# Performance work log

Measured on AMD Instinct MI355X. Metric: run time of the kernel, lower is better.

The kernel has to match this reference:

```python
import math
import jax, jax.numpy as jnp
import numpy as np

D_MODEL = 1024
HEAD_DIM = 64  # D_MODEL // NUM_HEADS
B, T = 8, 2048


def setup_inputs() -> dict:
    key = jax.random.key(0)
    k1, k2, k3, k4 = jax.random.split(key, 4)
    x = jax.random.normal(k1, (B, T, D_MODEL), dtype=jnp.float32)
    wq = jax.random.normal(k2, (D_MODEL, HEAD_DIM), dtype=jnp.float32) * (1.0 / math.sqrt(D_MODEL))
    wk = jax.random.normal(k3, (D_MODEL, HEAD_DIM), dtype=jnp.float32) * (1.0 / math.sqrt(D_MODEL))
    wv = jax.random.normal(k4, (D_MODEL, HEAD_DIM), dtype=jnp.float32) * (1.0 / math.sqrt(D_MODEL))
    return {"x": x, "wq": wq, "wk": wk, "wv": wv}


def reference(x, wq, wk, wv):
    # Single-head causal scaled dot-product attention (dropout = eval/identity).
    Tn = x.shape[1]
    q = jnp.einsum('btc,ch->bth', x, wq)  # [B,T,H]
    k = jnp.einsum('btc,ch->bth', x, wk)
    v = jnp.einsum('btc,ch->bth', x, wv)
    scale = 1.0 / math.sqrt(HEAD_DIM)
    scores = jnp.einsum('bth,bsh->bts', q, k) * scale  # [B,T,T]
    causal = jnp.tril(jnp.ones((Tn, Tn), dtype=bool))
    scores = jnp.where(causal, scores, -jnp.inf)
    weights = jax.nn.softmax(scores, axis=-1)
    return jnp.einsum('bts,bsh->bth', weights, v)  # [B,T,H]
```

## Files before the change

kernel.cpp:

```cpp
#include <hip/hip_runtime.h>

#define D_MODEL 1024
#define HDIM    64
#define BATCH   8
#define SEQ     2048
#define BT      (BATCH*SEQ)
#define NCAT    192
#define BM      32
#define BK      64
#define NSTEP   16
#define WFRAG   512
#define WSTEP32 (12*WFRAG)

typedef __attribute__((ext_vector_type(8))) short s8v;
typedef __attribute__((ext_vector_type(4))) float f4;

__device__ __forceinline__ unsigned short f2bf(float f){
    unsigned u = __builtin_bit_cast(unsigned, f);
    u += 0x7fffu + ((u >> 16) & 1u);
    return (unsigned short)(u >> 16);
}
__device__ __forceinline__ float bf2f(unsigned short h){
    unsigned u = ((unsigned)h) << 16;
    return __builtin_bit_cast(float, u);
}
__device__ __forceinline__ f4 MFMA(s8v a, s8v b, f4 c){
    return __builtin_amdgcn_mfma_f32_16x16x32_bf16(a, b, c, 0, 0, 0);
}

__global__ void prep_w_kernel(const float* __restrict__ wq, const float* __restrict__ wk,
                              const float* __restrict__ wv,
                              short* __restrict__ wtP){
    int ncat = blockIdx.x;
    const float* w = (ncat < 64) ? wq : ((ncat < 128) ? wk : wv);
    int n  = ncat & 63;
    int nb = ncat >> 4, ln = ncat & 15;
    for (int k = threadIdx.x; k < D_MODEL; k += blockDim.x){
        float f = w[k*HDIM + n];
        int t1 = k >> 5, g = (k >> 3) & 3, e = k & 7;
        wtP[(size_t)t1*WSTEP32 + (size_t)nb*WFRAG + ((g*16 + ln) << 3) + e]
            = (short)f2bf(f);
    }
}

__global__ __launch_bounds__(512, 4) void proj_kernel(
        const float* __restrict__ x,
        const short* __restrict__ wtP,
        short* __restrict__ q, short* __restrict__ k,
        short* __restrict__ vt){
    __shared__ __align__(16) float xs[4][BM][64];
    int tid = threadIdx.x;
    int wid = tid >> 6, lane = tid & 63, g = lane >> 4, ln = lane & 15;
    int wm = wid >> 2, wn = wid & 3;
    int m0 = blockIdx.x * BM;

    int srow = wid*4 + (lane >> 4);
    int sl   = lane & 15;
    int sswz = (sl & 8) | ((sl & 7) ^ (srow & 7));
    const float* xsrc = x + (size_t)(m0 + srow)*D_MODEL + sswz*4;
    const short* wb   = wtP + (size_t)(wn*3)*WFRAG + (size_t)lane*8;

    f4 acc[3];
#pragma unroll
    for (int i = 0; i < 3; i++) acc[i] = (f4){0.f,0.f,0.f,0.f};

    s8v wA0, wA1, wA2, wA3, wA4, wA5;
    s8v wB0, wB1, wB2, wB3, wB4, wB5;

#define GLOADX(T) { \
    __builtin_amdgcn_global_load_lds(xsrc + (size_t)(T)*BK, \
                                     &xs[(T) & 3][wid*4][0], 16, 0, 0); }

#define LOADW(P, T) { \
    const short* wp = wb + (size_t)(2*(T))*WSTEP32; \
    w##P##0 = *(const s8v*)(wp); \
    w##P##1 = *(const s8v*)(wp + WFRAG); \
    w##P##2 = *(const s8v*)(wp + 2*WFRAG); \
    w##P##3 = *(const s8v*)(wp + WSTEP32); \
    w##P##4 = *(const s8v*)(wp + WSTEP32 + WFRAG); \
    w##P##5 = *(const s8v*)(wp + WSTEP32 + 2*WFRAG); }

#define CVT8(DST, VA, VB) { \
    DST[0] = (short)f2bf(VA.x); DST[1] = (short)f2bf(VA.y); \
    DST[2] = (short)f2bf(VA.z); DST[3] = (short)f2bf(VA.w); \
    DST[4] = (short)f2bf(VB.x); DST[5] = (short)f2bf(VB.y); \
    DST[6] = (short)f2bf(VB.z); DST[7] = (short)f2bf(VB.w); }

#define STEP(P, T, VM) { \
    asm volatile("s_waitcnt vmcnt(" #VM ")" ::: "memory"); \
    __builtin_amdgcn_s_barrier(); \
    __builtin_amdgcn_sched_barrier(0); \
    int bq = (T) & 3, r = wm*16 + ln, r7 = ln & 7; \
    float4 xa = *(const float4*)&xs[bq][r][(((2*g)   ^ r7)) << 2]; \
    float4 xb = *(const float4*)&xs[bq][r][(((2*g+1) ^ r7)) << 2]; \
    float4 xc = *(const float4*)&xs[bq][r][((8 | ((2*g)   ^ r7))) << 2]; \
    float4 xd = *(const float4*)&xs[bq][r][((8 | ((2*g+1) ^ r7))) << 2]; \
    s8v A0, A1; \
    CVT8(A0, xa, xb) \
    CVT8(A1, xc, xd) \
    acc[0] = MFMA(A0, w##P##0, acc[0]); \
    acc[1] = MFMA(A0, w##P##1, acc[1]); \
    acc[2] = MFMA(A0, w##P##2, acc[2]); \
    acc[0] = MFMA(A1, w##P##3, acc[0]); \
    acc[1] = MFMA(A1, w##P##4, acc[1]); \
    acc[2] = MFMA(A1, w##P##5, acc[2]); \
    __builtin_amdgcn_sched_barrier(0); \
    if ((T) + 2 < NSTEP) LOADW(P, (T) + 2) \
    __builtin_amdgcn_sched_barrier(0); \
    if ((T) + 2 < NSTEP) GLOADX((T) + 2) \
    __builtin_amdgcn_sched_barrier(0); \
}

    LOADW(A, 0)
    __builtin_amdgcn_sched_barrier(0);
    GLOADX(0)
    __builtin_amdgcn_sched_barrier(0);
    LOADW(B, 1)
    __builtin_amdgcn_sched_barrier(0);
    GLOADX(1)
    __builtin_amdgcn_sched_barrier(0);

    for (int t = 0; t < 14; t += 2){
        STEP(A, t,     7)
        STEP(B, t + 1, 7)
    }
    STEP(A, 14, 7)
    STEP(B, 15, 0)
#undef GLOADX
#undef LOADW
#undef CVT8
#undef STEP

#pragma unroll
    for (int nb = 0; nb < 3; nb++){
        int ncat = wn*48 + nb*16 + ln;
        int mat = ncat >> 6, h = ncat & 63;
#pragma unroll
        for (int r = 0; r < 4; r++){
            size_t trow = (size_t)m0 + wm*16 + g*4 + r;
            float v = acc[nb][r];
            unsigned short hh = f2bf(v);
            if (mat == 0){
                q[trow*HDIM + h] = (short)hh;
            } else if (mat == 1){
                k[trow*HDIM + h] = (short)hh;
            } else {
                size_t bb = trow >> 11, t2 = trow & 2047;
                vt[((bb*HDIM + h) << 11) + t2] = (short)hh;
            }
        }
    }
}

__global__ __launch_bounds__(256, 5) void attn_kernel(
        const short* __restrict__ qg, const short* __restrict__ kg,
        const short* __restrict__ vt, float* __restrict__ out){
    __shared__ unsigned short plds[4][16][112];
    __shared__ float olds[4][16][65];
    __shared__ float mlds[4][16], llds[4][16];
    const float SC = 0.125f * 1.44269504088896340736f;
    int tid = threadIdx.x;
    int w = tid >> 6, lane = tid & 63, g = lane >> 4, ln = lane & 15;
    int b = blockIdx.y;
    int qi = ((blockIdx.y >> 1) & 1) ? (int)(gridDim.x - 1 - blockIdx.x) : (int)blockIdx.x;
    int tq = qi * 16;

    size_t qoff = ((size_t)b*SEQ + tq + ln) * HDIM + g*8;
    s8v q0 = *(const s8v*)(qg + qoff);
    s8v q1 = *(const s8v*)(qg + qoff + 32);

    f4 o0 = {0.f,0.f,0.f,0.f}, o1 = o0, o2 = o0, o3 = o0;
    float m[4], lsum[4];
#pragma unroll
    for (int r = 0; r < 4; r++){ m[r] = -__builtin_inff(); lsum[r] = 0.f; }

    int ntiles = (tq + 79) >> 6;
    for (int ti = w; ti < ntiles; ti += 4){
        int s0 = ti << 6;
        size_t kbase = ((size_t)b*SEQ + s0 + ln) * HDIM + g*8;
        f4 z0, z1, z2, z3;
#define QK_SUBTILE(ZJ, J) { \
        const short* kp = kg + kbase + (J)*16*HDIM; \
        s8v k0 = *(const s8v*)(kp); \
        s8v k1 = *(const s8v*)(kp + 32); \
        f4 s = {0.f,0.f,0.f,0.f}; \
        s = MFMA(q0, k0, s); s = MFMA(q1, k1, s); \
        ZJ[0] = s[0]*SC; ZJ[1] = s[1]*SC; ZJ[2] = s[2]*SC; ZJ[3] = s[3]*SC; }
        QK_SUBTILE(z0, 0)
        QK_SUBTILE(z1, 1)
        QK_SUBTILE(z2, 2)
        QK_SUBTILE(z3, 3)
#undef QK_SUBTILE
        if (s0 + 63 > tq){
#pragma unroll
            for (int r = 0; r < 4; r++){
                int t = tq + g*4 + r;
                if (s0      + ln > t) z0[r] = -__builtin_inff();
                if (s0 + 16 + ln > t) z1[r] = -__builtin_inff();
                if (s0 + 32 + ln > t) z2[r] = -__builtin_inff();
                if (s0 + 48 + ln > t) z3[r] = -__builtin_inff();
            }
        }
        float al[4];
#pragma unroll
        for (int r = 0; r < 4; r++){
            float v = fmaxf(fmaxf(z0[r], z1[r]), fmaxf(z2[r], z3[r]));
            v = fmaxf(v, __shfl_xor(v, 1));
            v = fmaxf(v, __shfl_xor(v, 2));
            v = fmaxf(v, __shfl_xor(v, 4));
            v = fmaxf(v, __shfl_xor(v, 8));
            float mn = fmaxf(m[r], v);
            al[r] = __builtin_amdgcn_exp2f(m[r] - mn);
            float p0 = __builtin_amdgcn_exp2f(z0[r] - mn);
            float p1 = __builtin_amdgcn_exp2f(z1[r] - mn);
            float p2 = __builtin_amdgcn_exp2f(z2[r] - mn);
            float p3 = __builtin_amdgcn_exp2f(z3[r] - mn);
            lsum[r] = lsum[r]*al[r] + ((p0 + p1) + (p2 + p3));
            m[r] = mn;
            int row = g*4 + r;
            plds[w][row][ln]      = f2bf(p0);
            plds[w][row][ln + 16] = f2bf(p1);
            plds[w][row][ln + 32] = f2bf(p2);
            plds[w][row][ln + 48] = f2bf(p3);
        }
#pragma unroll
        for (int r = 0; r < 4; r++){
            o0[r] *= al[r]; o1[r] *= al[r]; o2[r] *= al[r]; o3[r] *= al[r];
        }
        asm volatile("s_waitcnt lgkmcnt(0)" ::: "memory");
        __builtin_amdgcn_sched_barrier(0);
        s8v pa0 = *(const s8v*)&plds[w][ln][g*8];
        s8v pa1 = *(const s8v*)&plds[w][ln][32 + g*8];
        size_t voff = ((size_t)b*HDIM + ln) * SEQ + s0 + g*8;
        s8v v00 = *(const s8v*)(vt + voff);
        s8v v01 = *(const s8v*)(vt + voff + 32);
        s8v v10 = *(const s8v*)(vt + voff + 16*SEQ);
        s8v v11 = *(const s8v*)(vt + voff + 16*SEQ + 32);
        s8v v20 = *(const s8v*)(vt + voff + 32*SEQ);
        s8v v21 = *(const s8v*)(vt + voff + 32*SEQ + 32);
        s8v v30 = *(const s8v*)(vt + voff + 48*SEQ);
        s8v v31 = *(const s8v*)(vt + voff + 48*SEQ + 32);
        o0 = MFMA(pa0, v00, o0); o0 = MFMA(pa1, v01, o0);
        o1 = MFMA(pa0, v10, o1); o1 = MFMA(pa1, v11, o1);
        o2 = MFMA(pa0, v20, o2); o2 = MFMA(pa1, v21, o2);
        o3 = MFMA(pa0, v30, o3); o3 = MFMA(pa1, v31, o3);
    }

#pragma unroll
    for (int r = 0; r < 4; r++){
        float s = lsum[r];
        s += __shfl_xor(s, 1);
        s += __shfl_xor(s, 2);
        s += __shfl_xor(s, 4);
        s += __shfl_xor(s, 8);
        lsum[r] = s;
    }

#pragma unroll
    for (int r = 0; r < 4; r++){
        int row = g*4 + r;
        olds[w][row][ln]      = o0[r];
        olds[w][row][ln + 16] = o1[r];
        olds[w][row][ln + 32] = o2[r];
        olds[w][row][ln + 48] = o3[r];
        if (ln == 0){ mlds[w][row] = m[r]; llds[w][row] = lsum[r]; }
    }
    __syncthreads();

    {
        int row = tid >> 4;
        int hb  = tid & 15;
        float m0 = mlds[0][row], m1 = mlds[1][row], m2 = mlds[2][row], m3 = mlds[3][row];
        float M = fmaxf(fmaxf(m0, m1), fmaxf(m2, m3));
        float w0 = __builtin_amdgcn_exp2f(m0 - M);
        float w1 = __builtin_amdgcn_exp2f(m1 - M);
        float w2 = __builtin_amdgcn_exp2f(m2 - M);
        float w3 = __builtin_amdgcn_exp2f(m3 - M);
        float L = llds[0][row]*w0 + llds[1][row]*w1 + llds[2][row]*w2 + llds[3][row]*w3;
        float inv = 1.0f / L;
        size_t obase = ((size_t)b*SEQ + tq + row) * HDIM + hb;
#pragma unroll
        for (int j = 0; j < 4; j++){
            int h = hb + 16*j;
            float acc = olds[0][row][h]*w0 + olds[1][row][h]*w1
                      + olds[2][row][h]*w2 + olds[3][row][h]*w3;
            out[obase + 16*j] = acc * inv;
        }
    }
}

extern "C" void kernel_launch(void* const* d_in, const int* in_sizes, int n_in,
                              void* d_out, int out_size, void* d_ws, size_t ws_size,
                              hipStream_t stream) {
    (void)in_sizes; (void)n_in; (void)out_size; (void)ws_size;
    const float* x  = (const float*)d_in[0];
    const float* wq = (const float*)d_in[1];
    const float* wk = (const float*)d_in[2];
    const float* wv = (const float*)d_in[3];
    float* out = (float*)d_out;

    short* ws  = (short*)d_ws;
    short* wtP = ws;
    short* q   = wtP + (size_t)32*WSTEP32;
    short* k   = q + (size_t)BT*HDIM;
    short* vt  = k + (size_t)BT*HDIM;

    prep_w_kernel<<<NCAT, 256, 0, stream>>>(wq, wk, wv, wtP);
    proj_kernel<<<BT/BM, 512, 0, stream>>>(x, wtP, q, k, vt);
    attn_kernel<<<dim3(SEQ/16, BATCH), 256, 0, stream>>>(q, k, vt, out);
}
```

Baseline: 66.20 us.

## Stage projection weights in shared LDS and double the row tile

The projection kernel now uses 64-row tiles with 1024-thread blocks. Weight fragments are triple-buffered in LDS through global_load_lds issued by eight waves, instead of every wave loading its own weights into registers. This cuts redundant weight traffic from L2 and halves the number of blocks that each read the full weight matrix. In exchange, LDS use and block size grow, which limits occupancy, and each step adds LDS reads for the weight operands.

```diff
diff --git a/kernel.cpp b/kernel.cpp
--- a/kernel.cpp
+++ b/kernel.cpp
@@ -6,7 +6,7 @@
 #define SEQ     2048
 #define BT      (BATCH*SEQ)
 #define NCAT    192
-#define BM      32
+#define BM      64
 #define BK      64
 #define NSTEP   16
 #define WFRAG   512
@@ -43,42 +43,29 @@
     }
 }
 
-__global__ __launch_bounds__(512, 4) void proj_kernel(
+__global__ __launch_bounds__(1024) void proj_kernel(
         const float* __restrict__ x,
         const short* __restrict__ wtP,
         short* __restrict__ q, short* __restrict__ k,
         short* __restrict__ vt){
     __shared__ __align__(16) float xs[4][BM][64];
+    __shared__ __align__(16) short wlds[3][24][64][8];
     int tid = threadIdx.x;
     int wid = tid >> 6, lane = tid & 63, g = lane >> 4, ln = lane & 15;
     int wm = wid >> 2, wn = wid & 3;
     int m0 = blockIdx.x * BM;
 
-    int srow = wid*4 + (lane >> 4);
+    int rowA = (wid & 7)*8 + (lane >> 4), rowB = rowA + 4;
     int sl   = lane & 15;
-    int sswz = (sl & 8) | ((sl & 7) ^ (srow & 7));
-    const float* xsrc = x + (size_t)(m0 + srow)*D_MODEL + sswz*4;
-    const short* wb   = wtP + (size_t)(wn*3)*WFRAG + (size_t)lane*8;
+    int swzA = (sl & 8) | ((sl & 7) ^ (rowA & 7));
+    int swzB = (sl & 8) | ((sl & 7) ^ (rowB & 7));
+    const float* xsrcA = x + (size_t)(m0 + rowA)*D_MODEL + swzA*4;
+    const float* xsrcB = x + (size_t)(m0 + rowB)*D_MODEL + swzB*4;
+    const short* wsrc  = wtP + (size_t)(wid*3)*WFRAG + (size_t)lane*8;
 
     f4 acc[3];
 #pragma unroll
     for (int i = 0; i < 3; i++) acc[i] = (f4){0.f,0.f,0.f,0.f};
-
-    s8v wA0, wA1, wA2, wA3, wA4, wA5;
-    s8v wB0, wB1, wB2, wB3, wB4, wB5;
-
-#define GLOADX(T) { \
-    __builtin_amdgcn_global_load_lds(xsrc + (size_t)(T)*BK, \
-                                     &xs[(T) & 3][wid*4][0], 16, 0, 0); }
-
-#define LOADW(P, T) { \
-    const short* wp = wb + (size_t)(2*(T))*WSTEP32; \
-    w##P##0 = *(const s8v*)(wp); \
-    w##P##1 = *(const s8v*)(wp + WFRAG); \
-    w##P##2 = *(const s8v*)(wp + 2*WFRAG); \
-    w##P##3 = *(const s8v*)(wp + WSTEP32); \
-    w##P##4 = *(const s8v*)(wp + WSTEP32 + WFRAG); \
-    w##P##5 = *(const s8v*)(wp + WSTEP32 + 2*WFRAG); }
 
 #define CVT8(DST, VA, VB) { \
     DST[0] = (short)f2bf(VA.x); DST[1] = (short)f2bf(VA.y); \
@@ -86,11 +73,20 @@
     DST[4] = (short)f2bf(VB.x); DST[5] = (short)f2bf(VB.y); \
     DST[6] = (short)f2bf(VB.z); DST[7] = (short)f2bf(VB.w); }
 
-#define STEP(P, T, VM) { \
+#define GSTAGE(T) if (wid < 8){ \
+    const short* wp = wsrc + (size_t)(2*(T))*WSTEP32; \
+    __builtin_amdgcn_global_load_lds(wp,           &wlds[(T)%3][wid*3    ][0][0], 16, 0, 0); \
+    __builtin_amdgcn_global_load_lds(wp +   WFRAG, &wlds[(T)%3][wid*3 + 1][0][0], 16, 0, 0); \
+    __builtin_amdgcn_global_load_lds(wp + 2*WFRAG, &wlds[(T)%3][wid*3 + 2][0][0], 16, 0, 0); \
+    __builtin_amdgcn_global_load_lds(xsrcA + (size_t)(T)*BK, &xs[(T)&3][(wid&7)*8    ][0], 16, 0, 0); \
+    __builtin_amdgcn_global_load_lds(xsrcB + (size_t)(T)*BK, &xs[(T)&3][(wid&7)*8 + 4][0], 16, 0, 0); }
+
+#define STEP(T, VM) { \
     asm volatile("s_waitcnt vmcnt(" #VM ")" ::: "memory"); \
     __builtin_amdgcn_s_barrier(); \
     __builtin_amdgcn_sched_barrier(0); \
-    int bq = (T) & 3, r = wm*16 + ln, r7 = ln & 7; \
+    int bq = (T) & 3, wq = (T) % 3, r7 = ln & 7; \
+    int r = wm*16 + ln; \
     float4 xa = *(const float4*)&xs[bq][r][(((2*g)   ^ r7)) << 2]; \
     float4 xb = *(const float4*)&xs[bq][r][(((2*g+1) ^ r7)) << 2]; \
     float4 xc = *(const float4*)&xs[bq][r][((8 | ((2*g)   ^ r7))) << 2]; \
@@ -98,36 +94,33 @@
     s8v A0, A1; \
     CVT8(A0, xa, xb) \
     CVT8(A1, xc, xd) \
-    acc[0] = MFMA(A0, w##P##0, acc[0]); \
-    acc[1] = MFMA(A0, w##P##1, acc[1]); \
-    acc[2] = MFMA(A0, w##P##2, acc[2]); \
-    acc[0] = MFMA(A1, w##P##3, acc[0]); \
-    acc[1] = MFMA(A1, w##P##4, acc[1]); \
-    acc[2] = MFMA(A1, w##P##5, acc[2]); \
+    s8v B00 = *(const s8v*)&wlds[wq][     wn*3    ][lane][0]; \
+    s8v B01 = *(const s8v*)&wlds[wq][     wn*3 + 1][lane][0]; \
+    s8v B02 = *(const s8v*)&wlds[wq][     wn*3 + 2][lane][0]; \
+    s8v B10 = *(const s8v*)&wlds[wq][12 + wn*3    ][lane][0]; \
+    s8v B11 = *(const s8v*)&wlds[wq][12 + wn*3 + 1][lane][0]; \
+    s8v B12 = *(const s8v*)&wlds[wq][12 + wn*3 + 2][lane][0]; \
+    acc[0] = MFMA(A0, B00, acc[0]); \
+    acc[1] = MFMA(A0, B01, acc[1]); \
+    acc[2] = MFMA(A0, B02, acc[2]); \
+    acc[0] = MFMA(A1, B10, acc[0]); \
+    acc[1] = MFMA(A1, B11, acc[1]); \
+    acc[2] = MFMA(A1, B12, acc[2]); \
     __builtin_amdgcn_sched_barrier(0); \
-    if ((T) + 2 < NSTEP) LOADW(P, (T) + 2) \
+    if ((T) + 2 < NSTEP) GSTAGE((T) + 2) \
     __builtin_amdgcn_sched_barrier(0); \
-    if ((T) + 2 < NSTEP) GLOADX((T) + 2) \
-    __builtin_amdgcn_sched_barrier(0); \
-}
-
-    LOADW(A, 0)
+}
+
+    GSTAGE(0)
     __builtin_amdgcn_sched_barrier(0);
-    GLOADX(0)
+    GSTAGE(1)
     __builtin_amdgcn_sched_barrier(0);
-    LOADW(B, 1)
-    __builtin_amdgcn_sched_barrier(0);
-    GLOADX(1)
-    __builtin_amdgcn_sched_barrier(0);
-
-    for (int t = 0; t < 14; t += 2){
-        STEP(A, t,     7)
-        STEP(B, t + 1, 7)
-    }
-    STEP(A, 14, 7)
-    STEP(B, 15, 0)
-#undef GLOADX
-#undef LOADW
+
+    for (int t = 0; t < NSTEP - 1; ++t){
+        STEP(t, 5)
+    }
+    STEP(15, 0)
+#undef GSTAGE
 #undef CVT8
 #undef STEP
 
@@ -306,6 +299,6 @@
     short* vt  = k + (size_t)BT*HDIM;
 
     prep_w_kernel<<<NCAT, 256, 0, stream>>>(wq, wk, wv, wtP);
-    proj_kernel<<<BT/BM, 512, 0, stream>>>(x, wtP, q, k, vt);
+    proj_kernel<<<BT/BM, 1024, 0, stream>>>(x, wtP, q, k, vt);
     attn_kernel<<<dim3(SEQ/16, BATCH), 256, 0, stream>>>(q, k, vt, out);
 }
```

Measured after the change: 60.16 us. 1.1x faster.
